# Performance work log

Hardware: AMD Instinct MI355X
Metric: run time of the kernel (lower is better)

Reference implementation:

```python
import jax, jax.numpy as jnp
import numpy as np

H, HKV, HD = 16, 16, 64  # num_heads, num_kv_heads, head_dim

def rotate_half(x):
    x1, x2 = jnp.split(x, 2, axis=-1)
    return jnp.concatenate((-x2, x1), axis=-1)

def setup_inputs() -> dict:
    key = jax.random.key(0)
    ks = jax.random.split(key, 4)
    B, L, D = 4, 2048, 1024
    hidden_states = jax.random.normal(ks[0], (B, L, D), jnp.float32)
    # RoPE tables [L, head_dim]
    inv_freq = 1.0 / (10000.0 ** (jnp.arange(0, HD, 2, dtype=jnp.float32) / HD))
    freqs = jnp.outer(jnp.arange(L, dtype=jnp.float32), inv_freq)
    emb = jnp.concatenate((freqs, freqs), axis=-1)
    cos, sin = jnp.cos(emb), jnp.sin(emb)
    active_mask = jax.random.randint(ks[1], (B, L), 0, 2).astype(bool)
    Wqkv = jax.random.normal(ks[2], ((H + 2 * HKV) * HD, D), jnp.float32) / np.sqrt(D)
    Wo = jax.random.normal(ks[3], (D, H * HD), jnp.float32) / np.sqrt(H * HD)
    return {"hidden_states": hidden_states, "cos": cos, "sin": sin,
            "active_mask": active_mask, "Wqkv": Wqkv, "Wo": Wo}

def reference(hidden_states, cos, sin, active_mask, Wqkv, Wo):
    B, L, D = hidden_states.shape
    qkv = (hidden_states @ Wqkv.T).reshape(B, L, H + 2 * HKV, HD)
    q = qkv[:, :, :H]
    k = qkv[:, :, H:H + HKV]
    v = qkv[:, :, H + HKV:]
    c = cos[:, None, :]  # [L,1,HD] broadcasts over B and heads
    s = sin[:, None, :]
    q = q * c + rotate_half(q) * s
    k = k * c + rotate_half(k) * s
    # sparse queries: only active positions emit queries
    q = q * active_mask[:, :, None, None].astype(q.dtype)
    scale = 1.0 / np.sqrt(HD)
    scores = jnp.einsum('bqhd,bkhd->bhqk', q, k) * scale  # [B,H,L,L]
    attn = jax.nn.softmax(scores, axis=-1)
    out = jnp.einsum('bhqk,bkhd->bqhd', attn, v).reshape(B, L, H * HD)
    out = out @ Wo.T
    return out * active_mask[:, :, None].astype(out.dtype)
```

## Files before the change

### kernel.cpp

```cpp
#include <hip/hip_runtime.h>
#include <cstdint>

typedef _Float16 f16;
typedef __attribute__((ext_vector_type(2))) __fp16 fp16v2;
typedef __attribute__((ext_vector_type(4))) _Float16 f16x4;
typedef __attribute__((ext_vector_type(8))) _Float16 f16x8;
typedef __attribute__((ext_vector_type(4))) float f32x4;
typedef __attribute__((ext_vector_type(16))) float f32x16;

#if __has_builtin(__builtin_amdgcn_exp2f)
#define EXP2F(x) __builtin_amdgcn_exp2f(x)
#else
#define EXP2F(x) exp2f(x)
#endif

#if __has_builtin(__builtin_amdgcn_fdot2)
#define FDOT2(a, b, c) __builtin_amdgcn_fdot2((a), (b), (c), false)
#else
#define FDOT2(a, b, c) ((c) + (float)(a)[0] * (float)(b)[0] + (float)(a)[1] * (float)(b)[1])
#endif

#define GLOAD_LDS16(gp, lp) \
  __builtin_amdgcn_global_load_lds((const __attribute__((address_space(1))) void*)(gp), \
                                   (__attribute__((address_space(3))) void*)(lp), 16, 0, 0)

__global__ __launch_bounds__(256) void cvt_all(const float4* __restrict__ h, f16x4* __restrict__ h16,
                                               const float4* __restrict__ wq, f16x4* __restrict__ wq16,
                                               const float4* __restrict__ wo, f16x4* __restrict__ wo16,
                                               const float* __restrict__ cosb, const float* __restrict__ sinb,
                                               float2* __restrict__ cst) {
  int i = blockIdx.x * 256 + threadIdx.x;
  if (i >= 3145728) {
    const int i2 = i - 3145728;
    const int d = i2 >> 11, l = i2 & 2047;
    cst[i2] = make_float2(cosb[l * 64 + d], sinb[l * 64 + d]);
    return;
  }
  const float4* src;
  f16x4* dst;
  if (i < 2097152) { src = h + i; dst = h16 + i; }
  else if (i < 2883584) { src = wq + (i - 2097152); dst = wq16 + (i - 2097152); }
  else { src = wo + (i - 2883584); dst = wo16 + (i - 2883584); }
  float4 v = *src;
  f16x4 o;
  o.x = (f16)v.x; o.y = (f16)v.y; o.z = (f16)v.z; o.w = (f16)v.w;
  *dst = o;
}

template<int EPI, int N, int K>
__global__ __launch_bounds__(512) void gemm_bt2(
    const f16* __restrict__ A, const f16* __restrict__ Bm,
    f16* __restrict__ Qf, f16* __restrict__ Kf, f16* __restrict__ Vf,
    float* __restrict__ Cout, const int* __restrict__ mask,
    const float2* __restrict__ cst) {
  constexpr int NT = N / 128;
  constexpr int NKT = K / 64;
  const int tid = threadIdx.x;
  const int lane = tid & 63;
  const int wid = tid >> 6;
  const int wm = wid >> 1;
  const int wn = wid & 1;

  constexpr int nwg = 32 * NT;
  constexpr int cpx = nwg >> 3;
  const int swz = (blockIdx.x & 7) * cpx + (blockIdx.x >> 3);
  const int bm = swz / NT;
  const int bn = swz % NT;

  __shared__ f16 sA[2][256 * 64];
  __shared__ f16 sB[2][128 * 64];

  const f16* Abase = A + (size_t)bm * 256 * K;
  const f16* Bbase = Bm + (size_t)bn * 128 * K;

  f32x4 acc[4][4] = {};
  f16x8 af[4][2], bf[4][2];

  const int rowt = tid >> 3;
  const int c8 = (tid & 7) ^ (rowt & 7);
  const bool swp = (EPI == 1) && (bn < 16);

#define STAGE_KT(SLOT, KT)                                                      \
  do {                                                                          \
    _Pragma("unroll")                                                           \
    for (int g = 0; g < 4; ++g)                                                 \
      GLOAD_LDS16(Abase + (size_t)(g * 64 + rowt) * K + (KT) * 64 + c8 * 8,     \
                  &sA[SLOT][g * 4096 + tid * 8]);                               \
    _Pragma("unroll")                                                           \
    for (int g = 0; g < 2; ++g)                                                 \
      GLOAD_LDS16(Bbase + (size_t)(g * 64 + rowt) * K + (KT) * 64 + c8 * 8,     \
                  &sB[SLOT][g * 4096 + tid * 8]);                               \
  } while (0)

#define MFMA_CLUSTER(KS)                                                        \
  do {                                                                          \
    __builtin_amdgcn_s_setprio(1);                                              \
    if (swp) {                                                                  \
      _Pragma("unroll")                                                         \
      for (int i = 0; i < 4; ++i)                                               \
        _Pragma("unroll")                                                       \
        for (int j = 0; j < 4; ++j)                                             \
          acc[i][j] = __builtin_amdgcn_mfma_f32_16x16x32_f16(bf[i][KS], af[j][KS], acc[i][j], 0, 0, 0); \
    } else {                                                                    \
      _Pragma("unroll")                                                         \
      for (int i = 0; i < 4; ++i)                                               \
        _Pragma("unroll")                                                       \
        for (int j = 0; j < 4; ++j)                                             \
          acc[i][j] = __builtin_amdgcn_mfma_f32_16x16x32_f16(af[i][KS], bf[j][KS], acc[i][j], 0, 0, 0); \
    }                                                                           \
    __builtin_amdgcn_s_setprio(0);                                              \
  } while (0)

#define KTILE(VMC, DOSTAGE, KT, SLOT)                                           \
  do {                                                                          \
    asm volatile("s_waitcnt vmcnt(" #VMC ")" ::: "memory");                     \
    __builtin_amdgcn_s_barrier();                                               \
    __builtin_amdgcn_sched_barrier(0);                                          \
    _Pragma("unroll")                                                           \
    for (int i = 0; i < 4; ++i) {                                               \
      _Pragma("unroll")                                                         \
      for (int ks = 0; ks < 2; ++ks) {                                          \
        af[i][ks] = *(const f16x8*)&sA[SLOT][(wm * 64 + i * 16 + (lane & 15)) * 64 + ((ks * 4 + (lane >> 4)) ^ (lane & 7)) * 8]; \
        bf[i][ks] = *(const f16x8*)&sB[SLOT][(wn * 64 + i * 16 + (lane & 15)) * 64 + ((ks * 4 + (lane >> 4)) ^ (lane & 7)) * 8]; \
      }                                                                         \
    }                                                                           \
    MFMA_CLUSTER(0);                                                            \
    asm volatile("s_waitcnt lgkmcnt(0)" ::: "memory");                          \
    __builtin_amdgcn_sched_barrier(0);                                          \
    __builtin_amdgcn_s_barrier();                                               \
    if (DOSTAGE) { STAGE_KT(SLOT, (KT) + 2); }                                  \
    __builtin_amdgcn_sched_barrier(0);                                          \
    MFMA_CLUSTER(1);                                                            \
  } while (0)

  STAGE_KT(0, 0);
  STAGE_KT(1, 1);
#pragma unroll 1
  for (int it = 0; it < NKT - 2; it += 2) {
    KTILE(6, true, it, 0);
    KTILE(6, true, it + 1, 1);
  }
  KTILE(6, false, NKT - 2, 0);
  KTILE(0, false, NKT - 1, 1);

  const int lo = lane & 15;
  if constexpr (EPI == 1) {
    const int head = bn * 2 + wn;
    if (head < 32) {
      f16* dst = (head < 16) ? Qf : Kf;
      const int h15 = head & 15;
      const int h16l = lane >> 4;
      const int ahi = h16l >> 1, kkl = h16l & 1;
      #pragma unroll
      for (int j = 0; j < 4; ++j) {
        const int grow = bm * 256 + wm * 64 + j * 16 + lo;
        const int bb = grow >> 11, ll = grow & 2047;
        float msc = 1.0f;
        if (head < 16) msc = mask[bb * 2048 + ll] ? 0.18033688011112042f : 0.0f;
        f16* base = dst + (size_t)(bb * 16 + h15) * 64 * 2048;
        union { f16x8 v; fp16v2 hh[4]; } u0, u1;
        #pragma unroll
        for (int i = 0; i < 2; ++i) {
          float y0[4], y1[4];
          #pragma unroll
          for (int r = 0; r < 4; ++r) {
            const float2 cs = cst[(size_t)(i * 16 + 4 * h16l + r) * 2048 + ll];
            const float xl = acc[i][j][r], xh = acc[i + 2][j][r];
            y0[r] = (xl * cs.x - xh * cs.y) * msc;
            y1[r] = (xh * cs.x + xl * cs.y) * msc;
          }
          u0.hh[i * 2 + 0] = __builtin_amdgcn_cvt_pkrtz(y0[0], y0[1]);
          u0.hh[i * 2 + 1] = __builtin_amdgcn_cvt_pkrtz(y0[2], y0[3]);
          u1.hh[i * 2 + 0] = __builtin_amdgcn_cvt_pkrtz(y1[0], y1[1]);
          u1.hh[i * 2 + 1] = __builtin_amdgcn_cvt_pkrtz(y1[2], y1[3]);
        }
        const int t = ll >> 5, q5 = ll & 31;
        f16* p = base + (size_t)t * 2048 + (ahi * 32 + q5) * 8;
        *(f16x8*)(p + (kkl + 0) * 512) = u0.v;
        *(f16x8*)(p + (kkl + 2) * 512) = u1.v;
      }
    } else {
      const int hv = head - 32;
      #pragma unroll
      for (int i = 0; i < 4; ++i) {
        #pragma unroll
        for (int j = 0; j < 4; ++j) {
          #pragma unroll
          for (int r = 0; r < 4; ++r) {
            const int gm = bm * 256 + wm * 64 + i * 16 + (lane >> 4) * 4 + r;
            const int bb = gm >> 11, ll = gm & 2047;
            const int dd = j * 16 + lo;
            const int k = ll & 31;
            const int i32 = (k & ~12) | ((k & 4) << 1) | ((k & 8) >> 1);
            const int cc = i32 >> 4, hih = (i32 >> 3) & 1, jj = i32 & 7;
            const int blk = dd >> 5, qq = dd & 31;
            Vf[((size_t)(bb * 16 + hv) * 64 + (ll >> 5)) * 2048 +
               (cc * 2 + blk) * 512 + hih * 256 + qq * 8 + jj] = (f16)acc[i][j][r];
          }
        }
      }
    }
  } else {
    #pragma unroll
    for (int i = 0; i < 4; ++i) {
      #pragma unroll
      for (int j = 0; j < 4; ++j) {
        #pragma unroll
        for (int r = 0; r < 4; ++r) {
          const int gm = bm * 256 + wm * 64 + i * 16 + (lane >> 4) * 4 + r;
          const int gn = bn * 128 + wn * 64 + j * 16 + lo;
          const float mv = mask[gm] ? 1.0f : 0.0f;
          Cout[(size_t)gm * 1024 + gn] = acc[i][j][r] * mv;
        }
      }
    }
  }
#undef KTILE
#undef MFMA_CLUSTER
#undef STAGE_KT
}

#define LOADK(kd, kp)                                \
  do {                                               \
    _Pragma("unroll")                                \
    for (int _i = 0; _i < 4; ++_i)                   \
      kd[_i] = *(const f16x8*)&(kp)[_i * 512];       \
  } while (0)

#define QKBODY(SA, SB, kr)                                                       \
  do {                                                                           \
    __builtin_amdgcn_s_setprio(1);                                               \
    SA = __builtin_amdgcn_mfma_f32_32x32x16_f16(kr[0], qfa[0], z16, 0, 0, 0);    \
    SB = __builtin_amdgcn_mfma_f32_32x32x16_f16(kr[0], qfb[0], z16, 0, 0, 0);    \
    _Pragma("unroll")                                                            \
    for (int _k = 1; _k < 4; ++_k) {                                             \
      SA = __builtin_amdgcn_mfma_f32_32x32x16_f16(kr[_k], qfa[_k], SA, 0, 0, 0); \
      SB = __builtin_amdgcn_mfma_f32_32x32x16_f16(kr[_k], qfb[_k], SB, 0, 0, 0); \
    }                                                                            \
    __builtin_amdgcn_s_setprio(0);                                               \
  } while (0)

#define EXPPACK(SA, SB)                                                          \
  do {                                                                           \
    _Pragma("unroll")                                                            \
    for (int _i = 0; _i < 4; ++_i) {                                             \
      pa0.h[_i] = __builtin_amdgcn_cvt_pkrtz(EXP2F(SA[2 * _i]), EXP2F(SA[2 * _i + 1]));       \
      pa1.h[_i] = __builtin_amdgcn_cvt_pkrtz(EXP2F(SA[8 + 2 * _i]), EXP2F(SA[8 + 2 * _i + 1])); \
      la = FDOT2(pa0.h[_i], kOne, la);                                           \
      la = FDOT2(pa1.h[_i], kOne, la);                                           \
      pb0.h[_i] = __builtin_amdgcn_cvt_pkrtz(EXP2F(SB[2 * _i]), EXP2F(SB[2 * _i + 1]));       \
      pb1.h[_i] = __builtin_amdgcn_cvt_pkrtz(EXP2F(SB[8 + 2 * _i]), EXP2F(SB[8 + 2 * _i + 1])); \
      lb = FDOT2(pb0.h[_i], kOne, lb);                                           \
      lb = FDOT2(pb1.h[_i], kOne, lb);                                           \
    }                                                                            \
  } while (0)

#define PVBODY(vr)                                                               \
  do {                                                                           \
    __builtin_amdgcn_s_setprio(1);                                               \
    oa0 = __builtin_amdgcn_mfma_f32_32x32x16_f16(vr[0], pa0.v, oa0, 0, 0, 0);    \
    oa1 = __builtin_amdgcn_mfma_f32_32x32x16_f16(vr[1], pa0.v, oa1, 0, 0, 0);    \
    ob0 = __builtin_amdgcn_mfma_f32_32x32x16_f16(vr[0], pb0.v, ob0, 0, 0, 0);    \
    ob1 = __builtin_amdgcn_mfma_f32_32x32x16_f16(vr[1], pb0.v, ob1, 0, 0, 0);    \
    oa0 = __builtin_amdgcn_mfma_f32_32x32x16_f16(vr[2], pa1.v, oa0, 0, 0, 0);    \
    oa1 = __builtin_amdgcn_mfma_f32_32x32x16_f16(vr[3], pa1.v, oa1, 0, 0, 0);    \
    ob0 = __builtin_amdgcn_mfma_f32_32x32x16_f16(vr[2], pb1.v, ob0, 0, 0, 0);    \
    ob1 = __builtin_amdgcn_mfma_f32_32x32x16_f16(vr[3], pb1.v, ob1, 0, 0, 0);    \
    __builtin_amdgcn_s_setprio(0);                                               \
  } while (0)

__global__ __launch_bounds__(512) void attn_kernel(const f16* __restrict__ Qf,
                                                   const f16* __restrict__ Kf,
                                                   const f16* __restrict__ Vf,
                                                   f16* __restrict__ Ow) {
  const int bid = (blockIdx.x & 7) * 64 + (blockIdx.x >> 3);
  const int bh = bid >> 3;
  const int qt = bid & 7;
  const int lane = threadIdx.x & 63;
  const int wid = threadIdx.x >> 6;
  const int qw = wid & 3;
  const int kvh = wid >> 2;
  const int hi = lane >> 5;
  const int q = lane & 31;

  __shared__ float o_lds[8][32][65];
  __shared__ float l_lds[8][32];

  const f16* Qb = Qf + (size_t)bh * 64 * 2048;
  const f16* Kb = Kf + (size_t)bh * 64 * 2048;
  const f16* Vb = Vf + (size_t)bh * 64 * 2048;

  const int ta = qt * 8 + qw * 2;
  f16x8 qfa[4], qfb[4];
  {
    const f16* pa = Qb + (size_t)ta * 2048 + lane * 8;
    const f16* pb = pa + 2048;
    #pragma unroll
    for (int kk = 0; kk < 4; ++kk) {
      qfa[kk] = *(const f16x8*)&pa[kk * 512];
      qfb[kk] = *(const f16x8*)&pb[kk * 512];
    }
  }

  f32x16 oa0 = {}, oa1 = {}, ob0 = {}, ob1 = {};
  const f32x16 z16 = {};
  float la = 0.0f, lb = 0.0f;
  const fp16v2 kOne = {(__fp16)1.0f, (__fp16)1.0f};
  union PU { fp16v2 h[4]; f16x8 v; } pa0, pa1, pb0, pb1;

  const f16* kp = Kb + (size_t)(kvh * 32) * 2048 + lane * 8;
  const f16* vp = Vb + (size_t)(kvh * 32) * 2048 + lane * 8;
  f16x8 ka[4], kn[4], va[4], vn[4];
  f32x16 sa, sb, sa2, sb2;

  LOADK(ka, kp);  LOADK(va, vp);
  LOADK(kn, kp + 2048);  LOADK(vn, vp + 2048);
  QKBODY(sa, sb, ka);

#pragma unroll 1
  for (int t = 0; t < 30; t += 2) {
    EXPPACK(sa, sb);
    QKBODY(sa2, sb2, kn);
    LOADK(ka, kp + 4096);
    PVBODY(va);
    LOADK(va, vp + 4096);
    EXPPACK(sa2, sb2);
    QKBODY(sa, sb, ka);
    LOADK(kn, kp + 6144);
    PVBODY(vn);
    LOADK(vn, vp + 6144);
    kp += 4096; vp += 4096;
  }
  EXPPACK(sa, sb);
  QKBODY(sa2, sb2, kn);
  PVBODY(va);
  EXPPACK(sa2, sb2);
  PVBODY(vn);

  float lha = la + __shfl_xor(la, 32, 64);
  float lhb = lb + __shfl_xor(lb, 32, 64);

  if (kvh == 1) {
    #pragma unroll
    for (int blk = 0; blk < 2; ++blk)
      #pragma unroll
      for (int g = 0; g < 4; ++g)
        #pragma unroll
        for (int j = 0; j < 4; ++j) {
          const int d = blk * 32 + g * 8 + 4 * hi + j;
          o_lds[qw * 2 + 0][q][d] = blk ? oa1[g * 4 + j] : oa0[g * 4 + j];
          o_lds[qw * 2 + 1][q][d] = blk ? ob1[g * 4 + j] : ob0[g * 4 + j];
        }
    if (hi == 0) { l_lds[qw * 2 + 0][q] = lha; l_lds[qw * 2 + 1][q] = lhb; }
  }
  __syncthreads();
  if (kvh == 0) {
    const float inva = 1.0f / (lha + l_lds[qw * 2 + 0][q]);
    const float invb = 1.0f / (lhb + l_lds[qw * 2 + 1][q]);
    const int b = bh >> 4, h = bh & 15;
    const int qra = qt * 256 + qw * 64 + q;
    f16* orowa = Ow + ((size_t)(b * 2048 + qra)) * 1024 + h * 64;
    f16* orowb = orowa + 32 * 1024;
    #pragma unroll
    for (int blk = 0; blk < 2; ++blk) {
      #pragma unroll
      for (int g = 0; g < 4; ++g) {
        f16x4 sta, stb;
        #pragma unroll
        for (int j = 0; j < 4; ++j) {
          const int d = blk * 32 + g * 8 + 4 * hi + j;
          sta[j] = (f16)(((blk ? oa1[g * 4 + j] : oa0[g * 4 + j]) + o_lds[qw * 2 + 0][q][d]) * inva);
          stb[j] = (f16)(((blk ? ob1[g * 4 + j] : ob0[g * 4 + j]) + o_lds[qw * 2 + 1][q][d]) * invb);
        }
        *(f16x4*)&orowa[blk * 32 + g * 8 + 4 * hi] = sta;
        *(f16x4*)&orowb[blk * 32 + g * 8 + 4 * hi] = stb;
      }
    }
  }
}

extern "C" void kernel_launch(void* const* d_in, const int* in_sizes, int n_in,
                              void* d_out, int out_size, void* d_ws, size_t ws_size,
                              hipStream_t stream) {
  const float* hidden = (const float*)d_in[0];
  const float* cosb   = (const float*)d_in[1];
  const float* sinb   = (const float*)d_in[2];
  const int*   mask   = (const int*)d_in[3];
  const float* wqkv   = (const float*)d_in[4];
  const float* wo     = (const float*)d_in[5];
  float* out = (float*)d_out;
  char* ws = (char*)d_ws;

  f16* h16    = (f16*)(ws + 0);
  f16* wqkv16 = (f16*)(ws + 16777216);
  f16* wo16   = (f16*)(ws + 23068672);
  f16* Qfb    = (f16*)(ws + 25165824);
  f16* Kfb    = (f16*)(ws + 41943040);
  f16* Vfb    = (f16*)(ws + 58720256);
  float2* cst = (float2*)(ws + 75497472);
  f16* Ow     = h16;

  cvt_all<<<12544, 256, 0, stream>>>((const float4*)hidden, (f16x4*)h16,
                                     (const float4*)wqkv, (f16x4*)wqkv16,
                                     (const float4*)wo, (f16x4*)wo16,
                                     cosb, sinb, cst);

  gemm_bt2<1, 3072, 1024><<<768, 512, 0, stream>>>(h16, wqkv16, Qfb, Kfb, Vfb,
                                                   nullptr, mask, cst);

  attn_kernel<<<512, 512, 0, stream>>>(Qfb, Kfb, Vfb, Ow);

  gemm_bt2<2, 1024, 1024><<<256, 512, 0, stream>>>(Ow, wo16, nullptr, nullptr, nullptr,
                                                   out, mask, nullptr);
}
```

Before: 163.9 us.

## Stage K/V tiles through LDS with async global-to-LDS double buffering

Replaces per-wave direct global register loads of K and V with a block-cooperative global_load_lds double-buffered staging into shared memory. Each wave then reads its K/V fragments from LDS, with barriers between stages. The kernel previously had four query waves per KV half loading the same K/V data from global. The epilogue is also changed to exchange normalized fp16 partial outputs through a smaller LDS buffer to cut LDS footprint. This adds two barriers per tile and LDS read traffic, and the partial outputs now pass through fp16 rounding.

```diff
diff --git a/kernel.cpp b/kernel.cpp
--- a/kernel.cpp
+++ b/kernel.cpp
@@ -220,13 +220,6 @@
 #undef STAGE_KT
 }
 
-#define LOADK(kd, kp)                                \
-  do {                                               \
-    _Pragma("unroll")                                \
-    for (int _i = 0; _i < 4; ++_i)                   \
-      kd[_i] = *(const f16x8*)&(kp)[_i * 512];       \
-  } while (0)
-
 #define QKBODY(SA, SB, kr)                                                       \
   do {                                                                           \
     __builtin_amdgcn_s_setprio(1);                                               \
@@ -269,6 +262,35 @@
     __builtin_amdgcn_s_setprio(0);                                               \
   } while (0)
 
+#define ASTAGE(SLOT, T)                                                          \
+  do {                                                                           \
+    const f16* _s = sbase + (size_t)(T) * 2048;                                  \
+    GLOAD_LDS16(_s,       &sKV[SLOT][srgn][shh * 1024]);                         \
+    GLOAD_LDS16(_s + 512, &sKV[SLOT][srgn][shh * 1024 + 512]);                   \
+  } while (0)
+
+#define AKT(VMC, DOSTAGE, T, SLOT)                                               \
+  do {                                                                           \
+    asm volatile("s_waitcnt vmcnt(" #VMC ")" ::: "memory");                      \
+    __builtin_amdgcn_s_barrier();                                                \
+    __builtin_amdgcn_sched_barrier(0);                                           \
+    f16x8 kf[4], vf[4];                                                          \
+    _Pragma("unroll")                                                            \
+    for (int _k = 0; _k < 4; ++_k)                                               \
+      kf[_k] = *(const f16x8*)&sKV[SLOT][kvh * 2 + 0][_k * 512 + lane * 8];      \
+    _Pragma("unroll")                                                            \
+    for (int _c = 0; _c < 4; ++_c)                                               \
+      vf[_c] = *(const f16x8*)&sKV[SLOT][kvh * 2 + 1][_c * 512 + lane * 8];      \
+    QKBODY(sa, sb, kf);                                                          \
+    EXPPACK(sa, sb);                                                             \
+    asm volatile("s_waitcnt lgkmcnt(0)" ::: "memory");                           \
+    __builtin_amdgcn_sched_barrier(0);                                           \
+    __builtin_amdgcn_s_barrier();                                                \
+    if (DOSTAGE) { ASTAGE(SLOT, (T) + 2); }                                      \
+    __builtin_amdgcn_sched_barrier(0);                                           \
+    PVBODY(vf);                                                                  \
+  } while (0)
+
 __global__ __launch_bounds__(512) void attn_kernel(const f16* __restrict__ Qf,
                                                    const f16* __restrict__ Kf,
                                                    const f16* __restrict__ Vf,
@@ -283,8 +305,9 @@
   const int hi = lane >> 5;
   const int q = lane & 31;
 
-  __shared__ float o_lds[8][32][65];
-  __shared__ float l_lds[8][32];
+  __shared__ f16 sKV[2][4][2048];
+  __shared__ f16 o16[4][2][32][68];
+  __shared__ float l_lds[4][2][32];
 
   const f16* Qb = Qf + (size_t)bh * 64 * 2048;
   const f16* Kb = Kf + (size_t)bh * 64 * 2048;
@@ -302,61 +325,57 @@
     }
   }
 
+  const int srgn = wid >> 1;
+  const int shh = wid & 1;
+  const f16* sbase = ((srgn & 1) ? Vb : Kb) + (size_t)((srgn >> 1) * 32) * 2048 +
+                     shh * 1024 + lane * 8;
+
   f32x16 oa0 = {}, oa1 = {}, ob0 = {}, ob1 = {};
   const f32x16 z16 = {};
   float la = 0.0f, lb = 0.0f;
   const fp16v2 kOne = {(__fp16)1.0f, (__fp16)1.0f};
   union PU { fp16v2 h[4]; f16x8 v; } pa0, pa1, pb0, pb1;
-
-  const f16* kp = Kb + (size_t)(kvh * 32) * 2048 + lane * 8;
-  const f16* vp = Vb + (size_t)(kvh * 32) * 2048 + lane * 8;
-  f16x8 ka[4], kn[4], va[4], vn[4];
-  f32x16 sa, sb, sa2, sb2;
-
-  LOADK(ka, kp);  LOADK(va, vp);
-  LOADK(kn, kp + 2048);  LOADK(vn, vp + 2048);
-  QKBODY(sa, sb, ka);
-
+  f32x16 sa, sb;
+
+  ASTAGE(0, 0);
+  ASTAGE(1, 1);
 #pragma unroll 1
-  for (int t = 0; t < 30; t += 2) {
-    EXPPACK(sa, sb);
-    QKBODY(sa2, sb2, kn);
-    LOADK(ka, kp + 4096);
-    PVBODY(va);
-    LOADK(va, vp + 4096);
-    EXPPACK(sa2, sb2);
-    QKBODY(sa, sb, ka);
-    LOADK(kn, kp + 6144);
-    PVBODY(vn);
-    LOADK(vn, vp + 6144);
-    kp += 4096; vp += 4096;
-  }
-  EXPPACK(sa, sb);
-  QKBODY(sa2, sb2, kn);
-  PVBODY(va);
-  EXPPACK(sa2, sb2);
-  PVBODY(vn);
+  for (int t = 0; t < 28; t += 2) {
+    AKT(2, true, t, 0);
+    AKT(2, true, t + 1, 1);
+  }
+  AKT(2, true, 28, 0);
+  AKT(2, true, 29, 1);
+  AKT(2, false, 30, 0);
+  AKT(0, false, 31, 1);
 
   float lha = la + __shfl_xor(la, 32, 64);
   float lhb = lb + __shfl_xor(lb, 32, 64);
 
   if (kvh == 1) {
+    const float ia = 1.0f / lha, ib = 1.0f / lhb;
     #pragma unroll
     for (int blk = 0; blk < 2; ++blk)
       #pragma unroll
-      for (int g = 0; g < 4; ++g)
+      for (int g = 0; g < 4; ++g) {
+        f16x4 na, nb;
         #pragma unroll
         for (int j = 0; j < 4; ++j) {
-          const int d = blk * 32 + g * 8 + 4 * hi + j;
-          o_lds[qw * 2 + 0][q][d] = blk ? oa1[g * 4 + j] : oa0[g * 4 + j];
-          o_lds[qw * 2 + 1][q][d] = blk ? ob1[g * 4 + j] : ob0[g * 4 + j];
+          na[j] = (f16)((blk ? oa1[g * 4 + j] : oa0[g * 4 + j]) * ia);
+          nb[j] = (f16)((blk ? ob1[g * 4 + j] : ob0[g * 4 + j]) * ib);
         }
-    if (hi == 0) { l_lds[qw * 2 + 0][q] = lha; l_lds[qw * 2 + 1][q] = lhb; }
+        const int d = blk * 32 + g * 8 + 4 * hi;
+        *(f16x4*)&o16[qw][0][q][d] = na;
+        *(f16x4*)&o16[qw][1][q][d] = nb;
+      }
+    if (hi == 0) { l_lds[qw][0][q] = lha; l_lds[qw][1][q] = lhb; }
   }
   __syncthreads();
   if (kvh == 0) {
-    const float inva = 1.0f / (lha + l_lds[qw * 2 + 0][q]);
-    const float invb = 1.0f / (lhb + l_lds[qw * 2 + 1][q]);
+    const float l1a = l_lds[qw][0][q], l1b = l_lds[qw][1][q];
+    const float inva = 1.0f / (lha + l1a);
+    const float invb = 1.0f / (lhb + l1b);
+    const float w1a = l1a * inva, w1b = l1b * invb;
     const int b = bh >> 4, h = bh & 15;
     const int qra = qt * 256 + qw * 64 + q;
     f16* orowa = Ow + ((size_t)(b * 2048 + qra)) * 1024 + h * 64;
@@ -365,12 +384,14 @@
     for (int blk = 0; blk < 2; ++blk) {
       #pragma unroll
       for (int g = 0; g < 4; ++g) {
+        const int d = blk * 32 + g * 8 + 4 * hi;
+        const f16x4 na = *(const f16x4*)&o16[qw][0][q][d];
+        const f16x4 nb = *(const f16x4*)&o16[qw][1][q][d];
         f16x4 sta, stb;
         #pragma unroll
         for (int j = 0; j < 4; ++j) {
-          const int d = blk * 32 + g * 8 + 4 * hi + j;
-          sta[j] = (f16)(((blk ? oa1[g * 4 + j] : oa0[g * 4 + j]) + o_lds[qw * 2 + 0][q][d]) * inva);
-          stb[j] = (f16)(((blk ? ob1[g * 4 + j] : ob0[g * 4 + j]) + o_lds[qw * 2 + 1][q][d]) * invb);
+          sta[j] = (f16)((blk ? oa1[g * 4 + j] : oa0[g * 4 + j]) * inva + (float)na[j] * w1a);
+          stb[j] = (f16)((blk ? ob1[g * 4 + j] : ob0[g * 4 + j]) * invb + (float)nb[j] * w1b);
         }
         *(f16x4*)&orowa[blk * 32 + g * 8 + 4 * hi] = sta;
         *(f16x4*)&orowb[blk * 32 + g * 8 + 4 * hi] = stb;
```

After: 164.2 us. Within noise of the previous version (+0.2%).
